# Performance work log

Hardware: AMD Instinct MI355X
Metric: run time of the kernel (lower is better)

The kernel has to match this reference:

```python
import jax, jax.numpy as jnp
import numpy as np

B, S, DIM, H, DH = 1, 4096, 2048, 16, 128
EPS = 1e-5


def setup_inputs() -> dict:
    key = jax.random.key(0)
    ks = jax.random.split(key, 16)
    sc = 0.02
    inp = {
        'hidden_states': jax.random.normal(ks[0], (B, S, DIM), jnp.float32),
        'freqs_cos': jax.random.uniform(ks[1], (1, S, 1, DH), jnp.float32),
        'freqs_sin': jax.random.uniform(ks[2], (1, S, 1, DH), jnp.float32),
        'Wq': jax.random.normal(ks[3], (DIM, DIM), jnp.float32) * sc,
        'bq': jax.random.normal(ks[4], (DIM,), jnp.float32) * sc,
        'Wk': jax.random.normal(ks[5], (DIM, DIM), jnp.float32) * sc,
        'bk': jax.random.normal(ks[6], (DIM,), jnp.float32) * sc,
        'Wv': jax.random.normal(ks[7], (DIM, DIM), jnp.float32) * sc,
        'bv': jax.random.normal(ks[8], (DIM,), jnp.float32) * sc,
        'Wo': jax.random.normal(ks[9], (DIM, DIM), jnp.float32) * sc,
        'bo': jax.random.normal(ks[10], (DIM,), jnp.float32) * sc,
        'gq': jnp.ones((DIM,), jnp.float32),
        'gk': jnp.ones((DIM,), jnp.float32),
    }
    return inp


def _rmsnorm(x, g):
    var = jnp.mean(jnp.square(x), axis=-1, keepdims=True)
    return x * jax.lax.rsqrt(var + EPS) * g


def _apply_rope(x, freqs_cos, freqs_sin):
    # x: [B,S,H,DH]; interleaved rotary as in WanAttnProcessor
    x1 = x[..., 0::2]
    x2 = x[..., 1::2]
    cos = freqs_cos[..., 0::2]
    sin = freqs_sin[..., 1::2]
    o1 = x1 * cos - x2 * sin
    o2 = x1 * sin + x2 * cos
    return jnp.stack([o1, o2], axis=-1).reshape(x.shape)


def reference(hidden_states, freqs_cos, freqs_sin, Wq, bq, Wk, bk, Wv, bv, Wo, bo, gq, gk):
    q = hidden_states @ Wq + bq
    k = hidden_states @ Wk + bk
    v = hidden_states @ Wv + bv
    q = _rmsnorm(q, gq)
    k = _rmsnorm(k, gk)
    q = q.reshape(B, S, H, DH)
    k = k.reshape(B, S, H, DH)
    v = v.reshape(B, S, H, DH)
    q = _apply_rope(q, freqs_cos, freqs_sin)
    k = _apply_rope(k, freqs_cos, freqs_sin)
    scale = 1.0 / np.sqrt(DH).astype(np.float32)
    scores = jnp.einsum('bqhd,bkhd->bhqk', q, k) * scale
    attn = jax.nn.softmax(scores, axis=-1)
    out = jnp.einsum('bhqk,bkhd->bqhd', attn, v)
    out = out.reshape(B, S, H * DH)
    return out @ Wo + bo
```

## Files before the change

### kernel.cpp

```cpp
#include <hip/hip_runtime.h>

#define SEQ 4096
#define DIMC 2048
#define NH 16
#define DHD 128

typedef short s8v __attribute__((ext_vector_type(8)));
typedef float f4v __attribute__((ext_vector_type(4)));
typedef __bf16 bf8 __attribute__((ext_vector_type(8)));
typedef float f4 __attribute__((ext_vector_type(4)));

typedef __attribute__((address_space(3))) void lds_t;
typedef __attribute__((address_space(1))) void gbl_t;

__device__ __attribute__((aligned(256))) short g_h[(size_t)SEQ * DIMC];
__device__ __attribute__((aligned(256))) short g_q[(size_t)SEQ * DIMC];
__device__ __attribute__((aligned(256))) short g_k[(size_t)SEQ * DIMC];
__device__ __attribute__((aligned(256))) short g_v[(size_t)SEQ * DIMC];
__device__ __attribute__((aligned(256))) short g_vt[(size_t)DIMC * SEQ];
__device__ __attribute__((aligned(256))) short g_wt[4][(size_t)DIMC * DIMC];

__device__ __forceinline__ float b2f(short s) {
    union { unsigned u; float f; } v;
    v.u = ((unsigned)(unsigned short)s) << 16;
    return v.f;
}
__device__ __forceinline__ short f2b(float f) {
    union { float f; unsigned u; } v;
    v.f = f;
    unsigned b = v.u;
    b += 0x7FFFu + ((b >> 16) & 1u);
    return (short)(b >> 16);
}
__device__ __forceinline__ f4 mfma16(bf8 a, bf8 b, f4 c) {
    return __builtin_amdgcn_mfma_f32_16x16x32_bf16(a, b, c, 0, 0, 0);
}
__device__ __forceinline__ void gl_lds16(const short* g, short* l) {
    __builtin_amdgcn_global_load_lds((gbl_t*)g, (lds_t*)l, 16, 0, 0);
}

__global__ __launch_bounds__(256) void conv_h(const float* __restrict__ src) {
    size_t i = ((size_t)blockIdx.x * 256 + threadIdx.x) * 8;
    f4v u0 = *reinterpret_cast<const f4v*>(src + i);
    f4v u1 = *reinterpret_cast<const f4v*>(src + i + 4);
    s8v t;
    for (int j = 0; j < 4; ++j) { t[j] = f2b(u0[j]); t[4 + j] = f2b(u1[j]); }
    *reinterpret_cast<s8v*>(g_h + i) = t;
}

__global__ __launch_bounds__(256) void prep_w(const float* __restrict__ W0,
                                              const float* __restrict__ W1,
                                              const float* __restrict__ W2,
                                              const float* __restrict__ W3) {
    __shared__ __attribute__((aligned(16))) float t[64][68];
    const int z = blockIdx.z;
    const float* W = (z == 0) ? W0 : (z == 1) ? W1 : (z == 2) ? W2 : W3;
    short* WT = g_wt[z];
    const int r0 = blockIdx.y * 64, c0 = blockIdx.x * 64;
    const int tid = threadIdx.x;
    for (int i = 0; i < 4; ++i) {
        int slot = tid + i * 256;
        int r = slot >> 4, c4 = (slot & 15) * 4;
        *reinterpret_cast<f4v*>(&t[r][c4]) =
            *reinterpret_cast<const f4v*>(&W[(size_t)(r0 + r) * DIMC + c0 + c4]);
    }
    __syncthreads();
    for (int i = 0; i < 2; ++i) {
        int slot = tid + i * 256;
        int n = slot >> 3, k8 = (slot & 7) * 8;
        s8v o;
        for (int j = 0; j < 8; ++j) o[j] = f2b(t[k8 + j][n]);
        *reinterpret_cast<s8v*>(&WT[(size_t)(c0 + n) * DIMC + r0 + k8]) = o;
    }
}

template <int DSTF>
__device__ __forceinline__ void gemm_body(const short* __restrict__ X,
                                          const short* __restrict__ Bw,
                                          const float* __restrict__ bias,
                                          short* __restrict__ Yb,
                                          float* __restrict__ Yf,
                                          int bm, int bn) {
    __shared__ __attribute__((aligned(16))) short As[128 * 32];
    __shared__ __attribute__((aligned(16))) short Bs[128 * 32];
    const int tid = threadIdx.x;
    const int w = tid >> 6, lane = tid & 63;
    const int l16 = lane & 15, quad = lane >> 4;
    const int wm = w & 1, wn = w >> 1;

    f4 acc[4][4];
    for (int mi = 0; mi < 4; ++mi)
        for (int ni = 0; ni < 4; ++ni) acc[mi][ni] = (f4)0.0f;

    const int s0 = tid, s1 = tid + 256;
    const int ra0 = s0 >> 2, ca0 = (s0 & 3) * 8;
    const int ra1 = s1 >> 2, ca1 = (s1 & 3) * 8;
    const size_t xo0 = (size_t)(bm * 128 + ra0) * DIMC + ca0;
    const size_t xo1 = (size_t)(bm * 128 + ra1) * DIMC + ca1;
    const size_t bo0 = (size_t)(bn * 128 + ra0) * DIMC + ca0;
    const size_t bo1 = (size_t)(bn * 128 + ra1) * DIMC + ca1;
    short* lda0 = As + (size_t)(0 * 256 + w * 64) * 8;
    short* lda1 = As + (size_t)(1 * 256 + w * 64) * 8;
    short* ldb0 = Bs + (size_t)(0 * 256 + w * 64) * 8;
    short* ldb1 = Bs + (size_t)(1 * 256 + w * 64) * 8;

    for (int kb = 0; kb < DIMC; kb += 32) {
        __syncthreads();
        gl_lds16(X + xo0 + kb, lda0);
        gl_lds16(X + xo1 + kb, lda1);
        gl_lds16(Bw + bo0 + kb, ldb0);
        gl_lds16(Bw + bo1 + kb, ldb1);
        __syncthreads();
        bf8 af[4], bfr[4];
        for (int mi = 0; mi < 4; ++mi)
            af[mi] = *reinterpret_cast<const bf8*>(As + (wm * 64 + mi * 16 + l16) * 32 + quad * 8);
        for (int ni = 0; ni < 4; ++ni)
            bfr[ni] = *reinterpret_cast<const bf8*>(Bs + (wn * 64 + ni * 16 + l16) * 32 + quad * 8);
        for (int mi = 0; mi < 4; ++mi)
            for (int ni = 0; ni < 4; ++ni)
                acc[mi][ni] = mfma16(af[mi], bfr[ni], acc[mi][ni]);
    }

    for (int ni = 0; ni < 4; ++ni) {
        int col = bn * 128 + wn * 64 + ni * 16 + l16;
        float bcol = bias[col];
        for (int mi = 0; mi < 4; ++mi) {
            int row = bm * 128 + wm * 64 + mi * 16 + quad * 4;
            for (int r = 0; r < 4; ++r) {
                if (DSTF)
                    Yf[(size_t)(row + r) * DIMC + col] = acc[mi][ni][r] + bcol;
                else
                    Yb[(size_t)(row + r) * DIMC + col] = f2b(acc[mi][ni][r] + bcol);
            }
        }
    }
}

__global__ __launch_bounds__(256, 2) void gemm_qkv(const float* __restrict__ bq,
                                                   const float* __restrict__ bk,
                                                   const float* __restrict__ bv) {
    const int z = blockIdx.z;
    const float* bias = (z == 0) ? bq : (z == 1) ? bk : bv;
    short* Y = (z == 0) ? g_q : (z == 1) ? g_k : g_v;
    gemm_body<0>(g_h, g_wt[z], bias, Y, nullptr, blockIdx.y, blockIdx.x);
}

__global__ __launch_bounds__(256, 2) void gemm_o(const float* __restrict__ bias,
                                                 float* __restrict__ Yf) {
    gemm_body<1>(g_q, g_wt[3], bias, nullptr, Yf, blockIdx.y, blockIdx.x);
}

__global__ __launch_bounds__(256) void rmsnorm_rope(const float* __restrict__ gq,
                                                    const float* __restrict__ gk,
                                                    const float* __restrict__ fc,
                                                    const float* __restrict__ fs) {
    __shared__ float partial[4];
    __shared__ float totsh;
    const int s = blockIdx.x;
    const int which = blockIdx.y;
    short* x = which ? g_k : g_q;
    const float* g = which ? gk : gq;
    const int tid = threadIdx.x;
    const int d0 = tid * 8;

    s8v xv = *reinterpret_cast<const s8v*>(&x[(size_t)s * DIMC + d0]);
    float xf[8];
    float ssq = 0.0f;
    for (int j = 0; j < 8; ++j) { xf[j] = b2f(xv[j]); ssq += xf[j] * xf[j]; }
    for (int off = 32; off; off >>= 1) ssq += __shfl_down(ssq, off);
    if ((tid & 63) == 0) partial[tid >> 6] = ssq;
    __syncthreads();
    if (tid == 0) totsh = partial[0] + partial[1] + partial[2] + partial[3];
    __syncthreads();
    float rs = rsqrtf(totsh * (1.0f / (float)DIMC) + 1e-5f);
    if (which == 0) rs *= 0.12751744f;

    f4v g0 = *reinterpret_cast<const f4v*>(&g[d0]);
    f4v g1 = *reinterpret_cast<const f4v*>(&g[d0 + 4]);
    float xn[8];
    for (int j = 0; j < 4; ++j) { xn[j] = xf[j] * rs * g0[j]; xn[4 + j] = xf[4 + j] * rs * g1[j]; }

    s8v ov;
    for (int p = 0; p < 4; ++p) {
        int e = d0 + 2 * p;
        int hd = e & (DHD - 1);
        float c = fc[(size_t)s * DHD + hd];
        float sn = fs[(size_t)s * DHD + hd + 1];
        float x1 = xn[2 * p], x2 = xn[2 * p + 1];
        ov[2 * p]     = f2b(x1 * c - x2 * sn);
        ov[2 * p + 1] = f2b(x1 * sn + x2 * c);
    }
    *reinterpret_cast<s8v*>(&x[(size_t)s * DIMC + d0]) = ov;
}

__global__ __launch_bounds__(256) void transpose_v() {
    __shared__ __attribute__((aligned(16))) short t[64][72];
    const int h = blockIdx.z, dt = blockIdx.y, st = blockIdx.x;
    const int tid = threadIdx.x;
    const short* src = g_v + (size_t)st * 64 * DIMC + h * DHD + dt * 64;
    for (int i = 0; i < 2; ++i) {
        int slot = tid + i * 256;
        int s = slot >> 3, d8 = (slot & 7) * 8;
        *reinterpret_cast<s8v*>(&t[s][d8]) =
            *reinterpret_cast<const s8v*>(src + (size_t)s * DIMC + d8);
    }
    __syncthreads();
    short* dst = g_vt + (size_t)(h * DHD + dt * 64) * SEQ + st * 64;
    for (int i = 0; i < 2; ++i) {
        int slot = tid + i * 256;
        int d = slot >> 3, s8_ = (slot & 7) * 8;
        s8v o;
        for (int j = 0; j < 8; ++j) o[j] = t[s8_ + j][d];
        *reinterpret_cast<s8v*>(dst + (size_t)d * SEQ + s8_) = o;
    }
}

__global__ __launch_bounds__(256, 2) void attn_k() {
    __shared__ __attribute__((aligned(16))) short Ks0[64 * 128];
    __shared__ __attribute__((aligned(16))) short Vt0[128 * 64];
    __shared__ __attribute__((aligned(16))) float Ps[4][16][68];

    const int h = blockIdx.y;
    const int q0 = blockIdx.x * 128;
    const int tid = threadIdx.x;
    const int w = tid >> 6, lane = tid & 63;
    const int l16 = lane & 15, quad = lane >> 4;

    bf8 qf[2][4];
    for (int qs = 0; qs < 2; ++qs) {
        const short* qb = g_q + (size_t)(q0 + w * 32 + qs * 16 + l16) * DIMC + h * DHD + quad * 8;
        for (int c = 0; c < 4; ++c)
            qf[qs][c] = *reinterpret_cast<const bf8*>(qb + c * 32);
    }
    f4 of[2][8];
    for (int qs = 0; qs < 2; ++qs)
        for (int n = 0; n < 8; ++n) of[qs][n] = (f4)0.0f;
    float l4[2][4] = {{0.f, 0.f, 0.f, 0.f}, {0.f, 0.f, 0.f, 0.f}};

    const short* Kbase = g_k + h * DHD;
    const short* Vbase = g_vt + (size_t)h * DHD * SEQ;

    int krow[4], kcb[4], vd[4], vkb[4];
    for (int i = 0; i < 4; ++i) {
        int s = tid + i * 256;
        krow[i] = s >> 4; kcb[i] = ((s & 15) - krow[i]) & 15;
        vd[i] = s >> 3;   vkb[i] = ((s & 7) - vd[i]) & 7;
    }

    for (int kt = 0; kt < SEQ; kt += 64) {
        __syncthreads();
        for (int i = 0; i < 4; ++i)
            gl_lds16(Kbase + (size_t)(kt + krow[i]) * DIMC + kcb[i] * 8,
                     Ks0 + (size_t)(i * 256 + w * 64) * 8);
        for (int i = 0; i < 4; ++i)
            gl_lds16(Vbase + (size_t)vd[i] * SEQ + kt + vkb[i] * 8,
                     Vt0 + (size_t)(i * 256 + w * 64) * 8);
        __syncthreads();

        f4 sa[2][4];
        for (int qs = 0; qs < 2; ++qs)
            for (int ns = 0; ns < 4; ++ns) sa[qs][ns] = (f4)0.0f;
        for (int ns = 0; ns < 4; ++ns)
            for (int c = 0; c < 4; ++c) {
                bf8 kf = *reinterpret_cast<const bf8*>(
                    Ks0 + (ns * 16 + l16) * 128 + ((c * 4 + quad + l16) & 15) * 8);
                sa[0][ns] = mfma16(qf[0][c], kf, sa[0][ns]);
                sa[1][ns] = mfma16(qf[1][c], kf, sa[1][ns]);
            }

        bf8 pa[2][2];
        for (int qs = 0; qs < 2; ++qs) {
            for (int ns = 0; ns < 4; ++ns)
                for (int r = 0; r < 4; ++r) {
                    float p = exp2f(sa[qs][ns][r]);
                    Ps[w][quad * 4 + r][ns * 16 + l16] = p;
                    l4[qs][r] += p;
                }
            for (int c2 = 0; c2 < 2; ++c2) {
                const float* pp = &Ps[w][l16][c2 * 32 + quad * 8];
                s8v ps;
                for (int j = 0; j < 8; ++j) ps[j] = f2b(pp[j]);
                pa[qs][c2] = __builtin_bit_cast(bf8, ps);
            }
        }

        for (int c2 = 0; c2 < 2; ++c2)
            for (int n = 0; n < 8; ++n) {
                bf8 vf = *reinterpret_cast<const bf8*>(
                    Vt0 + (n * 16 + l16) * 64 + ((c2 * 4 + quad + l16) & 7) * 8);
                of[0][n] = mfma16(pa[0][c2], vf, of[0][n]);
                of[1][n] = mfma16(pa[1][c2], vf, of[1][n]);
            }
    }

    for (int qs = 0; qs < 2; ++qs)
        for (int r = 0; r < 4; ++r) {
            float ls = l4[qs][r];
            ls += __shfl_xor(ls, 1);
            ls += __shfl_xor(ls, 2);
            ls += __shfl_xor(ls, 4);
            ls += __shfl_xor(ls, 8);
            float inv = 1.0f / ls;
            int row = q0 + w * 32 + qs * 16 + quad * 4 + r;
            for (int n = 0; n < 8; ++n)
                g_q[(size_t)row * DIMC + h * DHD + n * 16 + l16] = f2b(of[qs][n][r] * inv);
        }
}

extern "C" void kernel_launch(void* const* d_in, const int* in_sizes, int n_in,
                              void* d_out, int out_size, void* d_ws, size_t ws_size,
                              hipStream_t stream) {
    const float* hidden = (const float*)d_in[0];
    const float* fc = (const float*)d_in[1];
    const float* fs = (const float*)d_in[2];
    const float* Wq = (const float*)d_in[3];
    const float* bq = (const float*)d_in[4];
    const float* Wk = (const float*)d_in[5];
    const float* bk = (const float*)d_in[6];
    const float* Wv = (const float*)d_in[7];
    const float* bv = (const float*)d_in[8];
    const float* Wo = (const float*)d_in[9];
    const float* bo = (const float*)d_in[10];
    const float* gq = (const float*)d_in[11];
    const float* gk = (const float*)d_in[12];

    dim3 blk(256);
    conv_h<<<dim3(4096), blk, 0, stream>>>(hidden);
    prep_w<<<dim3(32, 32, 4), blk, 0, stream>>>(Wq, Wk, Wv, Wo);
    gemm_qkv<<<dim3(16, 32, 3), blk, 0, stream>>>(bq, bk, bv);
    rmsnorm_rope<<<dim3(SEQ, 2), blk, 0, stream>>>(gq, gk, fc, fs);
    transpose_v<<<dim3(64, 2, NH), blk, 0, stream>>>();
    attn_k<<<dim3(32, NH), blk, 0, stream>>>();
    gemm_o<<<dim3(16, 32), blk, 0, stream>>>(bo, (float*)d_out);
}
```

Before: 571.0 us.

## Stage softmax probs as bf16 in LDS and compute row sums via MFMA

Converts the softmax probabilities to bf16 before writing them to the per-wave LDS scratch, halving LDS traffic and removing the per-element conversion after the reload. The row sums are now accumulated by an extra MFMA against a ones vector instead of scalar adds plus a final shuffle reduction, so the denominator uses the same bf16-rounded values as the numerator. K/V load addresses become incrementing pointers to cut per-iteration address arithmetic. The explicit full waitcnt before the LDS reload may serialize more than needed.

Result: faster. 559.4 us (-2.0%).

```diff
diff --git a/kernel.cpp b/kernel.cpp
--- a/kernel.cpp
+++ b/kernel.cpp
@@ -1,4 +1,5 @@
 #include <hip/hip_runtime.h>
+#include <hip/hip_bf16.h>
 
 #define SEQ 4096
 #define DIMC 2048
@@ -218,7 +219,7 @@
 __global__ __launch_bounds__(256, 2) void attn_k() {
     __shared__ __attribute__((aligned(16))) short Ks0[64 * 128];
     __shared__ __attribute__((aligned(16))) short Vt0[128 * 64];
-    __shared__ __attribute__((aligned(16))) float Ps[4][16][68];
+    __shared__ __attribute__((aligned(16))) __hip_bfloat16 Psb[4][16][72];
 
     const int h = blockIdx.y;
     const int q0 = blockIdx.x * 128;
@@ -235,26 +236,35 @@
     f4 of[2][8];
     for (int qs = 0; qs < 2; ++qs)
         for (int n = 0; n < 8; ++n) of[qs][n] = (f4)0.0f;
-    float l4[2][4] = {{0.f, 0.f, 0.f, 0.f}, {0.f, 0.f, 0.f, 0.f}};
+    f4 lacc[2] = {(f4)0.0f, (f4)0.0f};
+
+    s8v ob;
+    for (int j = 0; j < 8; ++j) ob[j] = (short)0x3F80;
+    const bf8 vones = __builtin_bit_cast(bf8, ob);
 
     const short* Kbase = g_k + h * DHD;
     const short* Vbase = g_vt + (size_t)h * DHD * SEQ;
 
-    int krow[4], kcb[4], vd[4], vkb[4];
+    const short* kp[4];
+    const short* vp[4];
     for (int i = 0; i < 4; ++i) {
         int s = tid + i * 256;
-        krow[i] = s >> 4; kcb[i] = ((s & 15) - krow[i]) & 15;
-        vd[i] = s >> 3;   vkb[i] = ((s & 7) - vd[i]) & 7;
+        int krow = s >> 4, kcb = ((s & 15) - krow) & 15;
+        int vd = s >> 3, vkb = ((s & 7) - vd) & 7;
+        kp[i] = Kbase + (size_t)krow * DIMC + kcb * 8;
+        vp[i] = Vbase + (size_t)vd * SEQ + vkb * 8;
     }
 
     for (int kt = 0; kt < SEQ; kt += 64) {
         __syncthreads();
-        for (int i = 0; i < 4; ++i)
-            gl_lds16(Kbase + (size_t)(kt + krow[i]) * DIMC + kcb[i] * 8,
-                     Ks0 + (size_t)(i * 256 + w * 64) * 8);
-        for (int i = 0; i < 4; ++i)
-            gl_lds16(Vbase + (size_t)vd[i] * SEQ + kt + vkb[i] * 8,
-                     Vt0 + (size_t)(i * 256 + w * 64) * 8);
+        for (int i = 0; i < 4; ++i) {
+            gl_lds16(kp[i], Ks0 + (size_t)(i * 256 + w * 64) * 8);
+            kp[i] += (size_t)64 * DIMC;
+        }
+        for (int i = 0; i < 4; ++i) {
+            gl_lds16(vp[i], Vt0 + (size_t)(i * 256 + w * 64) * 8);
+            vp[i] += 64;
+        }
         __syncthreads();
 
         f4 sa[2][4];
@@ -270,19 +280,28 @@
 
         bf8 pa[2][2];
         for (int qs = 0; qs < 2; ++qs) {
-            for (int ns = 0; ns < 4; ++ns)
-                for (int r = 0; r < 4; ++r) {
-                    float p = exp2f(sa[qs][ns][r]);
-                    Ps[w][quad * 4 + r][ns * 16 + l16] = p;
-                    l4[qs][r] += p;
-                }
-            for (int c2 = 0; c2 < 2; ++c2) {
-                const float* pp = &Ps[w][l16][c2 * 32 + quad * 8];
-                s8v ps;
-                for (int j = 0; j < 8; ++j) ps[j] = f2b(pp[j]);
-                pa[qs][c2] = __builtin_bit_cast(bf8, ps);
+            for (int ns = 0; ns < 4; ++ns) {
+                float p0 = exp2f(sa[qs][ns][0]);
+                float p1 = exp2f(sa[qs][ns][1]);
+                float p2 = exp2f(sa[qs][ns][2]);
+                float p3 = exp2f(sa[qs][ns][3]);
+                __hip_bfloat162 c01 = __float22bfloat162_rn({p0, p1});
+                __hip_bfloat162 c23 = __float22bfloat162_rn({p2, p3});
+                int col = ns * 16 + l16;
+                Psb[w][quad * 4 + 0][col] = c01.x;
+                Psb[w][quad * 4 + 1][col] = c01.y;
+                Psb[w][quad * 4 + 2][col] = c23.x;
+                Psb[w][quad * 4 + 3][col] = c23.y;
             }
-        }
+            __builtin_amdgcn_s_waitcnt(0);
+            for (int c2 = 0; c2 < 2; ++c2)
+                pa[qs][c2] = *reinterpret_cast<const bf8*>(&Psb[w][l16][c2 * 32 + quad * 8]);
+        }
+
+        lacc[0] = mfma16(pa[0][0], vones, lacc[0]);
+        lacc[0] = mfma16(pa[0][1], vones, lacc[0]);
+        lacc[1] = mfma16(pa[1][0], vones, lacc[1]);
+        lacc[1] = mfma16(pa[1][1], vones, lacc[1]);
 
         for (int c2 = 0; c2 < 2; ++c2)
             for (int n = 0; n < 8; ++n) {
@@ -295,12 +314,7 @@
 
     for (int qs = 0; qs < 2; ++qs)
         for (int r = 0; r < 4; ++r) {
-            float ls = l4[qs][r];
-            ls += __shfl_xor(ls, 1);
-            ls += __shfl_xor(ls, 2);
-            ls += __shfl_xor(ls, 4);
-            ls += __shfl_xor(ls, 8);
-            float inv = 1.0f / ls;
+            float inv = 1.0f / lacc[qs][r];
             int row = q0 + w * 32 + qs * 16 + quad * 4 + r;
             for (int n = 0; n < 8; ++n)
                 g_q[(size_t)row * DIMC + h * DHD + n * 16 + l16] = f2b(of[qs][n][r] * inv);
```
